# Kernel optimization log

Hardware: AMD Instinct MI355X
Metric: run time of the kernel (lower is better)

Reference implementation:

```python
import math
import jax, jax.numpy as jnp
import numpy as np

B, T, C = 8, 1024, 768
H = 12
D = C // H  # 64


def setup_inputs() -> dict:
    key = jax.random.key(0)
    k1, k2, k3, k4, k5 = jax.random.split(key, 5)
    s = 0.02
    return {
        "x": jax.random.normal(k1, (B, T, C), dtype=jnp.float32),
        "w_qkv": jax.random.normal(k2, (C, 3 * C), dtype=jnp.float32) * s,
        "b_qkv": jax.random.normal(k3, (3 * C,), dtype=jnp.float32) * s,
        "w_proj": jax.random.normal(k4, (C, C), dtype=jnp.float32) * s,
        "b_proj": jax.random.normal(k5, (C,), dtype=jnp.float32) * s,
    }


def reference(x, w_qkv, b_qkv, w_proj, b_proj):
    b, t, c = x.shape
    qkv = x @ w_qkv + b_qkv                      # [B,T,3C]
    q, k, v = jnp.split(qkv, 3, axis=-1)
    # [B,T,C] -> [B,H,T,D]
    q = q.reshape(b, t, H, D).transpose(0, 2, 1, 3)
    k = k.reshape(b, t, H, D).transpose(0, 2, 1, 3)
    v = v.reshape(b, t, H, D).transpose(0, 2, 1, 3)
    scale = 1.0 / math.sqrt(D)
    att = jnp.einsum("bhqd,bhkd->bhqk", q, k) * scale   # [B,H,T,T]
    causal = jnp.tril(jnp.ones((t, t), dtype=bool))
    att = jnp.where(causal, att, -jnp.inf)
    att = jax.nn.softmax(att, axis=-1)
    y = jnp.einsum("bhqk,bhkd->bhqd", att, v)            # [B,H,T,D]
    y = y.transpose(0, 2, 1, 3).reshape(b, t, c)
    return y @ w_proj + b_proj
```

## Files before the change

kernel.cpp:

```cpp
#include <hip/hip_runtime.h>
#include <math.h>

#define B_ 8
#define T_ 1024
#define C_ 768
#define H_ 12
#define D_ 64

typedef __bf16 bf16x8 __attribute__((ext_vector_type(8)));
typedef float  f32x4  __attribute__((ext_vector_type(4)));
typedef unsigned short us8 __attribute__((ext_vector_type(8)));
typedef unsigned int   u32x4v __attribute__((ext_vector_type(4)));

typedef __attribute__((address_space(3))) void lds_void;
typedef __attribute__((address_space(1))) const void glb_void;

#define KSC 0.18033688011112043f

__device__ __forceinline__ unsigned short f2bf(float f) {
    unsigned int u = __float_as_uint(f);
    u += 0x7fffu + ((u >> 16) & 1u);
    return (unsigned short)(u >> 16);
}

__global__ __launch_bounds__(256)
void prep_w(const float* __restrict__ x,
            const float* __restrict__ w_qkv, const float* __restrict__ b_qkv,
            const float* __restrict__ w_proj,
            unsigned short* __restrict__ wqT, unsigned short* __restrict__ wpT,
            float* __restrict__ bqs, unsigned short* __restrict__ xb) {
    __shared__ unsigned short Ts[64][65];
    const int id  = blockIdx.x;
    const int tid = threadIdx.x;
    if (id >= 577) {
        const int xid = id - 577;
        const float4* xi = (const float4*)x;
        ushort4* xo = (ushort4*)xb;
#pragma unroll
        for (int it = 0; it < 6; it++) {
            const int idx = (xid * 6 + it) * 256 + tid;
            float4 v = xi[idx];
            ushort4 o;
            o.x = f2bf(v.x); o.y = f2bf(v.y); o.z = f2bf(v.z); o.w = f2bf(v.w);
            xo[idx] = o;
        }
        return;
    }
    if (id == 576) {
        for (int i = tid; i < 3 * C_; i += 256)
            bqs[i] = b_qkv[i] * (i < C_ ? KSC : 1.f);
        return;
    }
    const float* W; unsigned short* Wt; int N, nlim, t2;
    if (id < 432) { t2 = id;       W = w_qkv;  Wt = wqT; N = 3 * C_; nlim = C_; }
    else          { t2 = id - 432; W = w_proj; Wt = wpT; N = C_;     nlim = 0;  }
    const int ntiles = N / 64;
    const int n0 = (t2 % ntiles) * 64, k0 = (t2 / ntiles) * 64;
    for (int i = tid; i < 4096; i += 256) {
        int n = i & 63, k = i >> 6;
        float sc = (n0 + n < nlim) ? KSC : 1.f;
        Ts[n][k] = f2bf(W[(size_t)(k0 + k) * N + n0 + n] * sc);
    }
    __syncthreads();
    for (int i = tid; i < 4096; i += 256) {
        int k = i & 63, n = i >> 6;
        Wt[(size_t)(n0 + n) * 768 + k0 + k] = Ts[n][k];
    }
}

template<int OUT_BF16>
__global__ __launch_bounds__(256, 3)
void gemm_big(const unsigned short* __restrict__ A16,
              const unsigned short* __restrict__ Bt, const float* __restrict__ bias,
              void* __restrict__ Cout, int M, int N, int K) {
    __shared__ __align__(16) unsigned short As[16384];
    __shared__ __align__(16) unsigned short Bs[6144];

    const int tid  = threadIdx.x;
    const int lane = tid & 63;
    const int c    = lane & 15;
    const int quad = lane >> 4;
    const int wave = tid >> 6;
    const int wm   = (wave >> 1) * 128;
    const int wn   = (wave & 1) * 48;
    const int bm   = blockIdx.x * 256;
    const int bn   = blockIdx.y * 96;

    const unsigned short* aS0;
    const unsigned short* bS0;
    {
        const int Lp = tid;
        const int L  = Lp ^ ((Lp >> 3) & 7);
        aS0 = A16 + (size_t)(bm + (L >> 3)) * K + (L & 7) * 8;
        bS0 = Bt  + (size_t)(bn + (L >> 3)) * K + (L & 7) * 8;
    }
    const int wb = (tid & 0xC0) * 8;

    int aoff[8][2], boff[3][2];
#pragma unroll
    for (int ks = 0; ks < 2; ks++) {
        const int kcA = (ks * 4 + quad) ^ (c & 7);
#pragma unroll
        for (int i = 0; i < 8; i++)
            aoff[i][ks] = ((wm + i * 16 + c) * 8 + kcA) * 8;
#pragma unroll
        for (int j = 0; j < 3; j++)
            boff[j][ks] = ((wn + j * 16 + c) * 8 + kcA) * 8;
    }

    f32x4 acc[8][3];
#pragma unroll
    for (int i = 0; i < 8; i++)
#pragma unroll
        for (int j = 0; j < 3; j++) acc[i][j] = (f32x4){0.f, 0.f, 0.f, 0.f};

#define STAGE_BIG()                                                            \
    {                                                                          \
        _Pragma("unroll")                                                      \
        for (int p = 0; p < 8; p++)                                            \
            __builtin_amdgcn_global_load_lds((glb_void*)(aS0 + (size_t)p * 32 * K), \
                (lds_void*)(&As[0] + p * 2048 + wb), 16, 0, 0);                \
        aS0 += 64;                                                             \
        _Pragma("unroll")                                                      \
        for (int p = 0; p < 3; p++)                                            \
            __builtin_amdgcn_global_load_lds((glb_void*)(bS0 + (size_t)p * 32 * K), \
                (lds_void*)(&Bs[0] + p * 2048 + wb), 16, 0, 0);                \
        bS0 += 64;                                                             \
    }

    STAGE_BIG()

    const int R = K >> 6;
    for (int r = 0; r < R; r++) {
        __syncthreads();

#pragma unroll
        for (int ks = 0; ks < 2; ks++) {
            bf16x8 bfr[3];
#pragma unroll
            for (int j = 0; j < 3; j++)
                bfr[j] = __builtin_bit_cast(bf16x8, *(const us8*)&Bs[boff[j][ks]]);
#pragma unroll
            for (int half = 0; half < 2; half++) {
                bf16x8 af[4];
#pragma unroll
                for (int i = 0; i < 4; i++)
                    af[i] = __builtin_bit_cast(bf16x8,
                        *(const us8*)&As[aoff[half * 4 + i][ks]]);
#pragma unroll
                for (int i = 0; i < 4; i++)
#pragma unroll
                    for (int j = 0; j < 3; j++)
                        acc[half * 4 + i][j] = __builtin_amdgcn_mfma_f32_16x16x32_bf16(
                            af[i], bfr[j], acc[half * 4 + i][j], 0, 0, 0);
            }
        }

        __syncthreads();

        if (r + 1 < R) STAGE_BIG()
    }
#undef STAGE_BIG

    float bs[3];
#pragma unroll
    for (int j = 0; j < 3; j++) bs[j] = bias[bn + wn + j * 16 + c];
#pragma unroll
    for (int i = 0; i < 8; i++) {
        const int gm = bm + wm + i * 16 + quad * 4;
#pragma unroll
        for (int r = 0; r < 4; r++) {
            const size_t ro = (size_t)(gm + r) * N;
#pragma unroll
            for (int j = 0; j < 3; j++) {
                const float v = acc[i][j][r] + bs[j];
                const int gn = bn + wn + j * 16 + c;
                if (OUT_BF16) ((unsigned short*)Cout)[ro + gn] = f2bf(v);
                else          ((float*)Cout)[ro + gn] = v;
            }
        }
    }
}

template<int OUT_BF16>
__global__ __launch_bounds__(256, 2)
void gemm_pipe(const unsigned short* __restrict__ A16,
               const unsigned short* __restrict__ Bt, const float* __restrict__ bias,
               void* __restrict__ Cout, int M, int N, int K) {
    __shared__ __align__(16) unsigned short As[8192];
    __shared__ __align__(16) unsigned short Bs[6144];

    const int tid  = threadIdx.x;
    const int lane = tid & 63;
    const int c    = lane & 15;
    const int quad = lane >> 4;
    const int wave = tid >> 6;
    const int wm   = (wave >> 1) * 64;
    const int wn   = (wave & 1) * 48;
    const int bm   = blockIdx.x * 128;
    const int bn   = blockIdx.y * 96;

    const unsigned short* aS[4];
    const unsigned short* bS[3];
#pragma unroll
    for (int p = 0; p < 4; p++) {
        const int Lp = p * 256 + tid;
        const int L  = Lp ^ ((Lp >> 3) & 7);
        aS[p] = A16 + (size_t)(bm + (L >> 3)) * K + (L & 7) * 8;
    }
#pragma unroll
    for (int p = 0; p < 3; p++) {
        const int Lp = p * 256 + tid;
        const int L  = Lp ^ ((Lp >> 3) & 7);
        bS[p] = Bt + (size_t)(bn + (L >> 3)) * K + (L & 7) * 8;
    }
    const int wb = (tid & 0xC0) * 8;

    int aoff[4][2], boff[3][2];
#pragma unroll
    for (int ks = 0; ks < 2; ks++) {
        const int kcA = (ks * 4 + quad) ^ (c & 7);
#pragma unroll
        for (int i = 0; i < 4; i++)
            aoff[i][ks] = ((wm + i * 16 + c) * 8 + kcA) * 8;
#pragma unroll
        for (int j = 0; j < 3; j++)
            boff[j][ks] = ((wn + j * 16 + c) * 8 + kcA) * 8;
    }

    f32x4 acc[4][3];
#pragma unroll
    for (int i = 0; i < 4; i++)
#pragma unroll
        for (int j = 0; j < 3; j++) acc[i][j] = (f32x4){0.f, 0.f, 0.f, 0.f};

#pragma unroll
    for (int p = 0; p < 4; p++) {
        __builtin_amdgcn_global_load_lds((glb_void*)aS[p],
            (lds_void*)(&As[0] + p * 2048 + wb), 16, 0, 0);
        aS[p] += 64;
    }
#pragma unroll
    for (int p = 0; p < 3; p++) {
        __builtin_amdgcn_global_load_lds((glb_void*)bS[p],
            (lds_void*)(&Bs[0] + p * 2048 + wb), 16, 0, 0);
        bS[p] += 64;
    }

    const int R = K >> 6;
    for (int r = 0; r < R; r++) {
        __syncthreads();

#pragma unroll
        for (int ks = 0; ks < 2; ks++) {
            bf16x8 af[4], bfr[3];
#pragma unroll
            for (int i = 0; i < 4; i++)
                af[i] = __builtin_bit_cast(bf16x8, *(const us8*)&As[aoff[i][ks]]);
#pragma unroll
            for (int j = 0; j < 3; j++)
                bfr[j] = __builtin_bit_cast(bf16x8, *(const us8*)&Bs[boff[j][ks]]);
#pragma unroll
            for (int i = 0; i < 4; i++)
#pragma unroll
                for (int j = 0; j < 3; j++)
                    acc[i][j] = __builtin_amdgcn_mfma_f32_16x16x32_bf16(af[i], bfr[j], acc[i][j], 0, 0, 0);
        }

        __syncthreads();

        if (r + 1 < R) {
#pragma unroll
            for (int p = 0; p < 4; p++) {
                __builtin_amdgcn_global_load_lds((glb_void*)aS[p],
                    (lds_void*)(&As[0] + p * 2048 + wb), 16, 0, 0);
                aS[p] += 64;
            }
#pragma unroll
            for (int p = 0; p < 3; p++) {
                __builtin_amdgcn_global_load_lds((glb_void*)bS[p],
                    (lds_void*)(&Bs[0] + p * 2048 + wb), 16, 0, 0);
                bS[p] += 64;
            }
        }
    }

    float bs[3];
#pragma unroll
    for (int j = 0; j < 3; j++) bs[j] = bias[bn + wn + j * 16 + c];
#pragma unroll
    for (int i = 0; i < 4; i++) {
        const int gm = bm + wm + i * 16 + quad * 4;
#pragma unroll
        for (int r = 0; r < 4; r++) {
            const size_t ro = (size_t)(gm + r) * N;
#pragma unroll
            for (int j = 0; j < 3; j++) {
                const float v = acc[i][j][r] + bs[j];
                const int gn = bn + wn + j * 16 + c;
                if (OUT_BF16) ((unsigned short*)Cout)[ro + gn] = f2bf(v);
                else          ((float*)Cout)[ro + gn] = v;
            }
        }
    }
}

__device__ __forceinline__ int sigmaK(int k) {
    return 16 * (2 * (k >> 5) + ((k >> 2) & 1)) + 4 * ((k >> 3) & 3) + (k & 3);
}

__global__ __launch_bounds__(256, 3)
void attn_mfma(const unsigned short* __restrict__ qkv, unsigned short* __restrict__ y) {
    __shared__ __align__(16) unsigned short Ks[64 * 72];
    __shared__ __align__(16) unsigned int   Vt[64 * 36];

    const int tid  = threadIdx.x;
    const int wave = tid >> 6;
    const int lane = tid & 63;
    const int c    = lane & 15;
    const int quad = lane >> 4;

    const int id = blockIdx.x;
    const int p  = (id >> 3) & 7;
    const int bh = (id >> 6) * 8 + (id & 7);
    const int b  = bh / H_;
    const int h  = bh - b * H_;

    const int qts[2] = {p, 15 - p};
    const int q0s[2] = {p * 64, (15 - p) * 64};

    const int RS = 3 * C_;
    const unsigned short* kbase = qkv + (size_t)b * T_ * RS + C_ + h * D_;
    const unsigned short* vbase = qkv + (size_t)b * T_ * RS + 2 * C_ + h * D_;

    const u32x4v onesu = {0x3F803F80u, 0x3F803F80u, 0x3F803F80u, 0x3F803F80u};
    const bf16x8 onesf = __builtin_bit_cast(bf16x8, onesu);

    bf16x8 qf[2][2];
#pragma unroll
    for (int t = 0; t < 2; t++) {
        const unsigned short* qrow =
            qkv + ((size_t)(b * T_ + q0s[t] + wave * 16 + c)) * RS + h * D_ + quad * 8;
        qf[t][0] = __builtin_bit_cast(bf16x8, *(const us8*)qrow);
        qf[t][1] = __builtin_bit_cast(bf16x8, *(const us8*)(qrow + 32));
    }

    const int kr0 = tid >> 3, kc0 = tid & 7;
    const int sK0 = sigmaK(kr0) * 72 + kc0 * 8;
    const int sK1 = sigmaK(kr0 + 32) * 72 + kc0 * 8;
    const int dg  = tid >> 4, kp0 = tid & 15;

    us8 kA, kB;
    ushort4 vA0, vB0, vA1, vB1;
    {
        kA = *(const us8*)(kbase + (size_t)kr0 * RS + kc0 * 8);
        kB = *(const us8*)(kbase + (size_t)(kr0 + 32) * RS + kc0 * 8);
        const unsigned short* p0 = vbase + (size_t)(2 * kp0) * RS + dg * 4;
        vA0 = *(const ushort4*)p0;  vB0 = *(const ushort4*)(p0 + RS);
        const unsigned short* p1 = vbase + (size_t)(2 * (kp0 + 16)) * RS + dg * 4;
        vA1 = *(const ushort4*)p1;  vB1 = *(const ushort4*)(p1 + RS);
    }

    f32x4 Oa[2][4];
    f32x4 Ol[2];
#pragma unroll
    for (int t = 0; t < 2; t++) {
        Ol[t] = (f32x4){0.f, 0.f, 0.f, 0.f};
#pragma unroll
        for (int d = 0; d < 4; d++) Oa[t][d] = (f32x4){0.f, 0.f, 0.f, 0.f};
    }

    const int ktEnd = qts[1];
    for (int kt = 0; kt <= ktEnd; kt++) {
        __syncthreads();
        *(us8*)&Ks[sK0] = kA;
        *(us8*)&Ks[sK1] = kB;
        {
            unsigned int* v0 = &Vt[(dg * 4) * 36 + kp0];
            v0[0]   = vA0.x | ((unsigned)vB0.x << 16);
            v0[36]  = vA0.y | ((unsigned)vB0.y << 16);
            v0[72]  = vA0.z | ((unsigned)vB0.z << 16);
            v0[108] = vA0.w | ((unsigned)vB0.w << 16);
            unsigned int* v1 = v0 + 16;
            v1[0]   = vA1.x | ((unsigned)vB1.x << 16);
            v1[36]  = vA1.y | ((unsigned)vB1.y << 16);
            v1[72]  = vA1.z | ((unsigned)vB1.z << 16);
            v1[108] = vA1.w | ((unsigned)vB1.w << 16);
        }
        __syncthreads();

        if (kt < ktEnd) {
            const unsigned short* kp = kbase + (size_t)((kt + 1) * 64) * RS;
            kA = *(const us8*)(kp + (size_t)kr0 * RS + kc0 * 8);
            kB = *(const us8*)(kp + (size_t)(kr0 + 32) * RS + kc0 * 8);
            const unsigned short* vp = vbase + (size_t)((kt + 1) * 64) * RS;
            const unsigned short* p0 = vp + (size_t)(2 * kp0) * RS + dg * 4;
            vA0 = *(const ushort4*)p0;  vB0 = *(const ushort4*)(p0 + RS);
            const unsigned short* p1 = vp + (size_t)(2 * (kp0 + 16)) * RS + dg * 4;
            vA1 = *(const ushort4*)p1;  vB1 = *(const ushort4*)(p1 + RS);
        }

        bf16x8 kf[4][2];
#pragma unroll
        for (int nb = 0; nb < 4; nb++) {
#pragma unroll
            for (int ks = 0; ks < 2; ks++)
                kf[nb][ks] = __builtin_bit_cast(bf16x8,
                    *(const us8*)&Ks[(nb * 16 + c) * 72 + quad * 8 + ks * 32]);
        }

#pragma unroll
        for (int t = 0; t < 2; t++) {
            if (kt > qts[t]) continue;
            const bool diag = (kt == qts[t]);
            const bool doHi = !diag || (wave >= 2);
            const int nbmax = diag ? ((wave >= 2) ? 3 : 1) : 3;

            f32x4 sv[4];
            __builtin_amdgcn_s_setprio(1);
#pragma unroll
            for (int nb = 0; nb < 4; nb++) {
                if (nb <= nbmax) {
                    f32x4 z = (f32x4){0.f, 0.f, 0.f, 0.f};
                    z = __builtin_amdgcn_mfma_f32_16x16x32_bf16(kf[nb][0], qf[t][0], z, 0, 0, 0);
                    sv[nb] = __builtin_amdgcn_mfma_f32_16x16x32_bf16(kf[nb][1], qf[t][1], z, 0, 0, 0);
                }
            }
            __builtin_amdgcn_s_setprio(0);
            if (diag) {
                const int qloc = wave * 16 + c;
#pragma unroll
                for (int nb = 0; nb < 4; nb++) {
                    if (nb <= nbmax) {
                        const int kb = 32 * (nb >> 1) + 4 * (nb & 1) + 8 * quad;
#pragma unroll
                        for (int r = 0; r < 4; r++)
                            if (kb + r > qloc) sv[nb][r] = -INFINITY;
                    }
                }
            }

            unsigned int pd[4][2];
#pragma unroll
            for (int nb = 0; nb < 4; nb++) {
                if (nb <= nbmax) {
                    float p0 = __builtin_amdgcn_exp2f(sv[nb][0]);
                    float p1 = __builtin_amdgcn_exp2f(sv[nb][1]);
                    float p2 = __builtin_amdgcn_exp2f(sv[nb][2]);
                    float p3 = __builtin_amdgcn_exp2f(sv[nb][3]);
                    unsigned u0 = __float_as_uint(p0) + 0x8000u;
                    unsigned u1 = __float_as_uint(p1) + 0x8000u;
                    unsigned u2 = __float_as_uint(p2) + 0x8000u;
                    unsigned u3 = __float_as_uint(p3) + 0x8000u;
                    pd[nb][0] = (u0 >> 16) | (u1 & 0xffff0000u);
                    pd[nb][1] = (u2 >> 16) | (u3 & 0xffff0000u);
                } else {
                    pd[nb][0] = 0u; pd[nb][1] = 0u;
                }
            }

            bf16x8 ap0 = __builtin_bit_cast(bf16x8,
                (u32x4v){pd[0][0], pd[0][1], pd[1][0], pd[1][1]});
            bf16x8 ap1 = __builtin_bit_cast(bf16x8,
                (u32x4v){pd[2][0], pd[2][1], pd[3][0], pd[3][1]});

            __builtin_amdgcn_s_setprio(1);
            Ol[t] = __builtin_amdgcn_mfma_f32_16x16x32_bf16(ap0, onesf, Ol[t], 0, 0, 0);
            if (doHi)
                Ol[t] = __builtin_amdgcn_mfma_f32_16x16x32_bf16(ap1, onesf, Ol[t], 0, 0, 0);

#pragma unroll
            for (int dd = 0; dd < 4; dd++) {
                const unsigned int* vrow = &Vt[(dd * 16 + c) * 36 + quad * 4];
                bf16x8 vb0 = __builtin_bit_cast(bf16x8, *(const u32x4v*)vrow);
                Oa[t][dd] = __builtin_amdgcn_mfma_f32_16x16x32_bf16(ap0, vb0, Oa[t][dd], 0, 0, 0);
                if (doHi) {
                    bf16x8 vb1 = __builtin_bit_cast(bf16x8, *(const u32x4v*)(vrow + 16));
                    Oa[t][dd] = __builtin_amdgcn_mfma_f32_16x16x32_bf16(ap1, vb1, Oa[t][dd], 0, 0, 0);
                }
            }
            __builtin_amdgcn_s_setprio(0);
        }
    }

#pragma unroll
    for (int t = 0; t < 2; t++) {
        unsigned short* yrow =
            y + ((size_t)(b * T_ + q0s[t] + wave * 16)) * C_ + h * D_;
#pragma unroll
        for (int r = 0; r < 4; r++) {
            float inv = 1.f / Ol[t][r];
#pragma unroll
            for (int dd = 0; dd < 4; dd++)
                yrow[(size_t)(quad * 4 + r) * C_ + dd * 16 + c] = f2bf(Oa[t][dd][r] * inv);
        }
    }
}

extern "C" void kernel_launch(void* const* d_in, const int* in_sizes, int n_in,
                              void* d_out, int out_size, void* d_ws, size_t ws_size,
                              hipStream_t stream) {
    const float* x      = (const float*)d_in[0];
    const float* w_qkv  = (const float*)d_in[1];
    const float* b_qkv  = (const float*)d_in[2];
    const float* w_proj = (const float*)d_in[3];
    const float* b_proj = (const float*)d_in[4];
    float* out = (float*)d_out;

    unsigned short* wqT  = (unsigned short*)d_ws;
    unsigned short* wpT  = wqT  + (size_t)3 * C_ * C_;
    unsigned short* qkvb = wpT  + (size_t)C_ * C_;
    unsigned short* yb   = qkvb + (size_t)B_ * T_ * 3 * C_;
    float*          bqs  = (float*)(yb + (size_t)B_ * T_ * C_);

    unsigned short* xb = yb;

    prep_w<<<1601, 256, 0, stream>>>(x, w_qkv, b_qkv, w_proj, wqT, wpT, bqs, xb);

    gemm_big<1><<<dim3(B_ * T_ / 256, 3 * C_ / 96), 256, 0, stream>>>(
        xb, wqT, bqs, qkvb, B_ * T_, 3 * C_, C_);

    attn_mfma<<<8 * B_ * H_, 256, 0, stream>>>(qkvb, yb);

    gemm_pipe<0><<<dim3(B_ * T_ / 128, C_ / 96), 256, 0, stream>>>(
        yb, wpT, b_proj, out, B_ * T_, C_, C_);
}
```

Baseline: 168.5 us.

## Split attention into one query tile per block with heaviest tiles scheduled first

The attention kernel previously paired query tile p with tile 15-p in each block so that per-block causal work was balanced. It now gives each block a single query tile, launches twice as many blocks in descending tile order so the longest blocks start first, and raises the launch-bounds occupancy hint from 3 to 4. The goal is more parallelism and lower register pressure. The cost is that K/V tiles shared by the paired queries are now loaded from global memory and staged into LDS twice.

```diff
diff --git a/kernel.cpp b/kernel.cpp
--- a/kernel.cpp
+++ b/kernel.cpp
@@ -309,7 +309,7 @@
     return 16 * (2 * (k >> 5) + ((k >> 2) & 1)) + 4 * ((k >> 3) & 3) + (k & 3);
 }
 
-__global__ __launch_bounds__(256, 3)
+__global__ __launch_bounds__(256, 4)
 void attn_mfma(const unsigned short* __restrict__ qkv, unsigned short* __restrict__ y) {
     __shared__ __align__(16) unsigned short Ks[64 * 72];
     __shared__ __align__(16) unsigned int   Vt[64 * 36];
@@ -321,13 +321,11 @@
     const int quad = lane >> 4;
 
     const int id = blockIdx.x;
-    const int p  = (id >> 3) & 7;
-    const int bh = (id >> 6) * 8 + (id & 7);
+    const int bh = (id >> 7) * 8 + (id & 7);
+    const int qt = 15 - ((id >> 3) & 15);
     const int b  = bh / H_;
     const int h  = bh - b * H_;
-
-    const int qts[2] = {p, 15 - p};
-    const int q0s[2] = {p * 64, (15 - p) * 64};
+    const int q0 = qt * 64;
 
     const int RS = 3 * C_;
     const unsigned short* kbase = qkv + (size_t)b * T_ * RS + C_ + h * D_;
@@ -336,13 +334,12 @@
     const u32x4v onesu = {0x3F803F80u, 0x3F803F80u, 0x3F803F80u, 0x3F803F80u};
     const bf16x8 onesf = __builtin_bit_cast(bf16x8, onesu);
 
-    bf16x8 qf[2][2];
-#pragma unroll
-    for (int t = 0; t < 2; t++) {
+    bf16x8 qf[2];
+    {
         const unsigned short* qrow =
-            qkv + ((size_t)(b * T_ + q0s[t] + wave * 16 + c)) * RS + h * D_ + quad * 8;
-        qf[t][0] = __builtin_bit_cast(bf16x8, *(const us8*)qrow);
-        qf[t][1] = __builtin_bit_cast(bf16x8, *(const us8*)(qrow + 32));
+            qkv + ((size_t)(b * T_ + q0 + wave * 16 + c)) * RS + h * D_ + quad * 8;
+        qf[0] = __builtin_bit_cast(bf16x8, *(const us8*)qrow);
+        qf[1] = __builtin_bit_cast(bf16x8, *(const us8*)(qrow + 32));
     }
 
     const int kr0 = tid >> 3, kc0 = tid & 7;
@@ -361,17 +358,12 @@
         vA1 = *(const ushort4*)p1;  vB1 = *(const ushort4*)(p1 + RS);
     }
 
-    f32x4 Oa[2][4];
-    f32x4 Ol[2];
-#pragma unroll
-    for (int t = 0; t < 2; t++) {
-        Ol[t] = (f32x4){0.f, 0.f, 0.f, 0.f};
-#pragma unroll
-        for (int d = 0; d < 4; d++) Oa[t][d] = (f32x4){0.f, 0.f, 0.f, 0.f};
-    }
-
-    const int ktEnd = qts[1];
-    for (int kt = 0; kt <= ktEnd; kt++) {
+    f32x4 Oa[4];
+    f32x4 Ol = (f32x4){0.f, 0.f, 0.f, 0.f};
+#pragma unroll
+    for (int d = 0; d < 4; d++) Oa[d] = (f32x4){0.f, 0.f, 0.f, 0.f};
+
+    for (int kt = 0; kt <= qt; kt++) {
         __syncthreads();
         *(us8*)&Ks[sK0] = kA;
         *(us8*)&Ks[sK1] = kB;
@@ -389,7 +381,7 @@
         }
         __syncthreads();
 
-        if (kt < ktEnd) {
+        if (kt < qt) {
             const unsigned short* kp = kbase + (size_t)((kt + 1) * 64) * RS;
             kA = *(const us8*)(kp + (size_t)kr0 * RS + kc0 * 8);
             kB = *(const us8*)(kp + (size_t)(kr0 + 32) * RS + kc0 * 8);
@@ -409,90 +401,85 @@
                     *(const us8*)&Ks[(nb * 16 + c) * 72 + quad * 8 + ks * 32]);
         }
 
-#pragma unroll
-        for (int t = 0; t < 2; t++) {
-            if (kt > qts[t]) continue;
-            const bool diag = (kt == qts[t]);
-            const bool doHi = !diag || (wave >= 2);
-            const int nbmax = diag ? ((wave >= 2) ? 3 : 1) : 3;
-
-            f32x4 sv[4];
-            __builtin_amdgcn_s_setprio(1);
+        const bool diag = (kt == qt);
+        const bool doHi = !diag || (wave >= 2);
+        const int nbmax = diag ? ((wave >= 2) ? 3 : 1) : 3;
+
+        f32x4 sv[4];
+        __builtin_amdgcn_s_setprio(1);
+#pragma unroll
+        for (int nb = 0; nb < 4; nb++) {
+            if (nb <= nbmax) {
+                f32x4 z = (f32x4){0.f, 0.f, 0.f, 0.f};
+                z = __builtin_amdgcn_mfma_f32_16x16x32_bf16(kf[nb][0], qf[0], z, 0, 0, 0);
+                sv[nb] = __builtin_amdgcn_mfma_f32_16x16x32_bf16(kf[nb][1], qf[1], z, 0, 0, 0);
+            }
+        }
+        __builtin_amdgcn_s_setprio(0);
+        if (diag) {
+            const int qloc = wave * 16 + c;
 #pragma unroll
             for (int nb = 0; nb < 4; nb++) {
                 if (nb <= nbmax) {
-                    f32x4 z = (f32x4){0.f, 0.f, 0.f, 0.f};
-                    z = __builtin_amdgcn_mfma_f32_16x16x32_bf16(kf[nb][0], qf[t][0], z, 0, 0, 0);
-                    sv[nb] = __builtin_amdgcn_mfma_f32_16x16x32_bf16(kf[nb][1], qf[t][1], z, 0, 0, 0);
+                    const int kb = 32 * (nb >> 1) + 4 * (nb & 1) + 8 * quad;
+#pragma unroll
+                    for (int r = 0; r < 4; r++)
+                        if (kb + r > qloc) sv[nb][r] = -INFINITY;
                 }
             }
-            __builtin_amdgcn_s_setprio(0);
-            if (diag) {
-                const int qloc = wave * 16 + c;
-#pragma unroll
-                for (int nb = 0; nb < 4; nb++) {
-                    if (nb <= nbmax) {
-                        const int kb = 32 * (nb >> 1) + 4 * (nb & 1) + 8 * quad;
-#pragma unroll
-                        for (int r = 0; r < 4; r++)
-                            if (kb + r > qloc) sv[nb][r] = -INFINITY;
-                    }
-                }
-            }
-
-            unsigned int pd[4][2];
-#pragma unroll
-            for (int nb = 0; nb < 4; nb++) {
-                if (nb <= nbmax) {
-                    float p0 = __builtin_amdgcn_exp2f(sv[nb][0]);
-                    float p1 = __builtin_amdgcn_exp2f(sv[nb][1]);
-                    float p2 = __builtin_amdgcn_exp2f(sv[nb][2]);
-                    float p3 = __builtin_amdgcn_exp2f(sv[nb][3]);
-                    unsigned u0 = __float_as_uint(p0) + 0x8000u;
-                    unsigned u1 = __float_as_uint(p1) + 0x8000u;
-                    unsigned u2 = __float_as_uint(p2) + 0x8000u;
-                    unsigned u3 = __float_as_uint(p3) + 0x8000u;
-                    pd[nb][0] = (u0 >> 16) | (u1 & 0xffff0000u);
-                    pd[nb][1] = (u2 >> 16) | (u3 & 0xffff0000u);
-                } else {
-                    pd[nb][0] = 0u; pd[nb][1] = 0u;
-                }
-            }
-
-            bf16x8 ap0 = __builtin_bit_cast(bf16x8,
-                (u32x4v){pd[0][0], pd[0][1], pd[1][0], pd[1][1]});
-            bf16x8 ap1 = __builtin_bit_cast(bf16x8,
-                (u32x4v){pd[2][0], pd[2][1], pd[3][0], pd[3][1]});
-
-            __builtin_amdgcn_s_setprio(1);
-            Ol[t] = __builtin_amdgcn_mfma_f32_16x16x32_bf16(ap0, onesf, Ol[t], 0, 0, 0);
-            if (doHi)
-                Ol[t] = __builtin_amdgcn_mfma_f32_16x16x32_bf16(ap1, onesf, Ol[t], 0, 0, 0);
-
-#pragma unroll
-            for (int dd = 0; dd < 4; dd++) {
-                const unsigned int* vrow = &Vt[(dd * 16 + c) * 36 + quad * 4];
-                bf16x8 vb0 = __builtin_bit_cast(bf16x8, *(const u32x4v*)vrow);
-                Oa[t][dd] = __builtin_amdgcn_mfma_f32_16x16x32_bf16(ap0, vb0, Oa[t][dd], 0, 0, 0);
-                if (doHi) {
-                    bf16x8 vb1 = __builtin_bit_cast(bf16x8, *(const u32x4v*)(vrow + 16));
-                    Oa[t][dd] = __builtin_amdgcn_mfma_f32_16x16x32_bf16(ap1, vb1, Oa[t][dd], 0, 0, 0);
-                }
-            }
-            __builtin_amdgcn_s_setprio(0);
-        }
-    }
-
-#pragma unroll
-    for (int t = 0; t < 2; t++) {
+        }
+
+        unsigned int pd[4][2];
+#pragma unroll
+        for (int nb = 0; nb < 4; nb++) {
+            if (nb <= nbmax) {
+                float p0 = __builtin_amdgcn_exp2f(sv[nb][0]);
+                float p1 = __builtin_amdgcn_exp2f(sv[nb][1]);
+                float p2 = __builtin_amdgcn_exp2f(sv[nb][2]);
+                float p3 = __builtin_amdgcn_exp2f(sv[nb][3]);
+                unsigned u0 = __float_as_uint(p0) + 0x8000u;
+                unsigned u1 = __float_as_uint(p1) + 0x8000u;
+                unsigned u2 = __float_as_uint(p2) + 0x8000u;
+                unsigned u3 = __float_as_uint(p3) + 0x8000u;
+                pd[nb][0] = (u0 >> 16) | (u1 & 0xffff0000u);
+                pd[nb][1] = (u2 >> 16) | (u3 & 0xffff0000u);
+            } else {
+                pd[nb][0] = 0u; pd[nb][1] = 0u;
+            }
+        }
+
+        bf16x8 ap0 = __builtin_bit_cast(bf16x8,
+            (u32x4v){pd[0][0], pd[0][1], pd[1][0], pd[1][1]});
+        bf16x8 ap1 = __builtin_bit_cast(bf16x8,
+            (u32x4v){pd[2][0], pd[2][1], pd[3][0], pd[3][1]});
+
+        __builtin_amdgcn_s_setprio(1);
+        Ol = __builtin_amdgcn_mfma_f32_16x16x32_bf16(ap0, onesf, Ol, 0, 0, 0);
+        if (doHi)
+            Ol = __builtin_amdgcn_mfma_f32_16x16x32_bf16(ap1, onesf, Ol, 0, 0, 0);
+
+#pragma unroll
+        for (int dd = 0; dd < 4; dd++) {
+            const unsigned int* vrow = &Vt[(dd * 16 + c) * 36 + quad * 4];
+            bf16x8 vb0 = __builtin_bit_cast(bf16x8, *(const u32x4v*)vrow);
+            Oa[dd] = __builtin_amdgcn_mfma_f32_16x16x32_bf16(ap0, vb0, Oa[dd], 0, 0, 0);
+            if (doHi) {
+                bf16x8 vb1 = __builtin_bit_cast(bf16x8, *(const u32x4v*)(vrow + 16));
+                Oa[dd] = __builtin_amdgcn_mfma_f32_16x16x32_bf16(ap1, vb1, Oa[dd], 0, 0, 0);
+            }
+        }
+        __builtin_amdgcn_s_setprio(0);
+    }
+
+    {
         unsigned short* yrow =
-            y + ((size_t)(b * T_ + q0s[t] + wave * 16)) * C_ + h * D_;
+            y + ((size_t)(b * T_ + q0 + wave * 16)) * C_ + h * D_;
 #pragma unroll
         for (int r = 0; r < 4; r++) {
-            float inv = 1.f / Ol[t][r];
+            float inv = 1.f / Ol[r];
 #pragma unroll
             for (int dd = 0; dd < 4; dd++)
-                yrow[(size_t)(quad * 4 + r) * C_ + dd * 16 + c] = f2bf(Oa[t][dd][r] * inv);
+                yrow[(size_t)(quad * 4 + r) * C_ + dd * 16 + c] = f2bf(Oa[dd][r] * inv);
         }
     }
 }
@@ -520,7 +507,7 @@
     gemm_big<1><<<dim3(B_ * T_ / 256, 3 * C_ / 96), 256, 0, stream>>>(
         xb, wqT, bqs, qkvb, B_ * T_, 3 * C_, C_);
 
-    attn_mfma<<<8 * B_ * H_, 256, 0, stream>>>(qkvb, yb);
+    attn_mfma<<<16 * B_ * H_, 256, 0, stream>>>(qkvb, yb);
 
     gemm_pipe<0><<<dim3(B_ * T_ / 128, C_ / 96), 256, 0, stream>>>(
         yb, wpT, b_proj, out, B_ * T_, C_, C_);
```

After: 177.4 us. 1.05x slower.
